# Kernel optimization log

Measured on AMD Instinct MI355X. Metric: run time of the kernel, lower is better.

The kernel has to match this reference:

```python
import jax, jax.numpy as jnp
import numpy as np

N = 50000        # nodes
E = 1_600_000    # edges (avg degree 32)
DIN, DH, DOUT = 128, 128, 64
TAU = 0.5
EPS = 1e-12
BN_EPS = 1e-5


def _lin(key, din, dout):
    kw, kb = jax.random.split(key)
    s = 1.0 / np.sqrt(din)
    W = jax.random.uniform(kw, (din, dout), jnp.float32, -s, s)
    b = jax.random.uniform(kb, (dout,), jnp.float32, -s, s)
    return W, b


def setup_inputs() -> dict:
    key = jax.random.key(0)
    ks = jax.random.split(key, 12)
    x = jax.random.normal(ks[0], (N, DIN), jnp.float32)
    edge_index = jax.random.randint(ks[1], (2, E), 0, N, dtype=jnp.int32).astype(jnp.int64)
    Wn0, cn0 = _lin(ks[2], DIN, DH)
    Wr0, cr0 = _lin(ks[3], DIN, DH)
    Wn1, cn1 = _lin(ks[4], DH, DH)
    Wr1, cr1 = _lin(ks[5], DH, DH)
    Wn2, cn2 = _lin(ks[6], DH, DOUT)
    Wr2, cr2 = _lin(ks[7], DH, DOUT)
    g0 = jnp.ones((DH,), jnp.float32); b0 = jnp.zeros((DH,), jnp.float32)
    m0 = 0.1 * jax.random.normal(ks[8], (DH,), jnp.float32)
    v0 = jax.random.uniform(ks[9], (DH,), jnp.float32, 0.5, 1.5)
    g1 = jnp.ones((DH,), jnp.float32); b1 = jnp.zeros((DH,), jnp.float32)
    m1 = 0.1 * jax.random.normal(ks[10], (DH,), jnp.float32)
    v1 = jax.random.uniform(ks[11], (DH,), jnp.float32, 0.5, 1.5)
    return dict(x=x, edge_index=edge_index,
                Wn0=Wn0, cn0=cn0, Wr0=Wr0, cr0=cr0,
                Wn1=Wn1, cn1=cn1, Wr1=Wr1, cr1=cr1,
                Wn2=Wn2, cn2=cn2, Wr2=Wr2, cr2=cr2,
                g0=g0, b0=b0, m0=m0, v0=v0,
                g1=g1, b1=b1, m1=m1, v1=v1)


def _edge_weights(x_sim, src, dst):
    # cosine similarity per edge, then softmax over incoming edges of each dst
    xn = x_sim / (jnp.linalg.norm(x_sim, axis=-1, keepdims=True) + EPS)
    sim = jnp.sum(xn[src] * xn[dst], axis=-1)            # [E]
    logits = sim / max(TAU, EPS)
    m = jax.ops.segment_max(logits, dst, num_segments=N)
    m = jnp.where(jnp.isfinite(m), m, 0.0)               # empty segments
    e = jnp.exp(logits - m[dst])
    denom = jax.ops.segment_sum(e, dst, num_segments=N)
    return e / (denom[dst] + 1e-16)


def _conv(x, src, dst, w, Wn, cn, Wr, cr):
    # gather x[src], scale by edge weight, scatter-add into dst
    agg = jax.ops.segment_sum(x[src] * w[:, None], dst, num_segments=N)  # [N, d]
    return agg @ Wn + cn + x @ Wr + cr


def _bn_eval(h, g, b, m, v):
    return (h - m) * (g / jnp.sqrt(v + BN_EPS)) + b


def reference(x, edge_index, Wn0, cn0, Wr0, cr0, Wn1, cn1, Wr1, cr1,
              Wn2, cn2, Wr2, cr2, g0, b0, m0, v0, g1, b1, m1, v1):
    src, dst = edge_index[0], edge_index[1]
    w = _edge_weights(x, src, dst)
    h = _conv(x, src, dst, w, Wn0, cn0, Wr0, cr0)
    h = jax.nn.relu(_bn_eval(h, g0, b0, m0, v0))
    h = _conv(h, src, dst, w, Wn1, cn1, Wr1, cr1)
    h = jax.nn.relu(_bn_eval(h, g1, b1, m1, v1))
    return _conv(h, src, dst, w, Wn2, cn2, Wr2, cr2)
```

## Files before the change

kernel.cpp:

```cpp
#include <hip/hip_runtime.h>
#include <hip/hip_fp16.h>
#include <hip/hip_fp8.h>
#include <math.h>
#include <type_traits>

#define N_NODES 50000
#define E_EDGES 1600000
#define TAU     0.5f
#define BN_EPS  1e-5f
#define SBSH    9
#define NSB     ((N_NODES + 511) >> 9)
#define NSUBL   8
#define SUBCAP  2560
#define BINCAP  48
#define EPB     1024
#define SCGRID  ((E_EDGES + EPB - 1) / EPB)
#define BSTR    16

typedef _Float16 f16x8 __attribute__((ext_vector_type(8)));
typedef float    f32x4 __attribute__((ext_vector_type(4)));
typedef float    f32x2 __attribute__((ext_vector_type(2)));

__device__ __forceinline__ f32x2 pk_fma(f32x2 a, f32x2 b, f32x2 c) {
  f32x2 d;
  asm volatile("v_pk_fma_f32 %0, %1, %2, %3"
               : "=v"(d) : "v"(a), "v"(b), "v"(c));
  return d;
}

__device__ __forceinline__ float dot16_fp8(int4 a, int4 b) {
  unsigned wa[4] = {(unsigned)a.x, (unsigned)a.y, (unsigned)a.z, (unsigned)a.w};
  unsigned wb[4] = {(unsigned)b.x, (unsigned)b.y, (unsigned)b.z, (unsigned)b.w};
  float acc = 0.0f;
  #pragma unroll
  for (int i = 0; i < 4; ++i) {
    f32x2 alo = __builtin_amdgcn_cvt_pk_f32_fp8(wa[i], false);
    f32x2 ahi = __builtin_amdgcn_cvt_pk_f32_fp8(wa[i], true);
    f32x2 blo = __builtin_amdgcn_cvt_pk_f32_fp8(wb[i], false);
    f32x2 bhi = __builtin_amdgcn_cvt_pk_f32_fp8(wb[i], true);
    acc = fmaf(alo[0], blo[0], acc);
    acc = fmaf(alo[1], blo[1], acc);
    acc = fmaf(ahi[0], bhi[0], acc);
    acc = fmaf(ahi[1], bhi[1], acc);
  }
  return acc;
}

__global__ __launch_bounds__(256) void xn_norm(
    const float* __restrict__ x, unsigned char* __restrict__ xn8, int n) {
  int wid  = (int)((blockIdx.x * blockDim.x + threadIdx.x) >> 6);
  int lane = threadIdx.x & 63;
  if (wid >= n) return;
  float2 v = ((const float2*)(x + (size_t)wid * 128))[lane];
  float s = v.x * v.x + v.y * v.y;
  #pragma unroll
  for (int off = 32; off; off >>= 1) s += __shfl_xor(s, off);
  float inv = 1.0f / (sqrtf(s) + 1e-12f);
  __hip_fp8_e4m3 q0(v.x * inv), q1(v.y * inv);
  uchar2 pk;
  pk.x = q0.__x; pk.y = q1.__x;
  ((uchar2*)(xn8 + (size_t)wid * 128))[lane] = pk;
}

__global__ __launch_bounds__(256) void scatter_sb(
    const int* __restrict__ src, const int* __restrict__ dst,
    int* __restrict__ gc, unsigned* __restrict__ staging,
    int* __restrict__ ocnt, unsigned* __restrict__ ostage, int e) {
  __shared__ unsigned bins[NSB][BINCAP];
  __shared__ int bcount[NSB];
  const int tid  = threadIdx.x;
  const int wv   = tid >> 6;
  const int lane = tid & 63;
  const int sl   = blockIdx.x & (NSUBL - 1);
  for (int i = tid; i < NSB; i += 256) bcount[i] = 0;
  __syncthreads();

  int base = blockIdx.x * EPB;
  int bend = min(base + EPB, e);
  for (int i = base + tid; i < bend; i += 256) {
    int d = dst[i], s = src[i];
    int sb = d >> SBSH;
    int pos = atomicAdd(&bcount[sb], 1);
    if (pos < BINCAP) {
      bins[sb][pos] = (unsigned)s | ((unsigned)(d & 511) << 16);
    } else {
      int op = atomicAdd(ocnt, 1);
      ostage[op] = (unsigned)s | ((unsigned)d << 16);
    }
  }
  __syncthreads();

  for (int sb = wv; sb < NSB; sb += 4) {
    int cnt = min(bcount[sb], BINCAP);
    if (cnt > 0) {
      int cell = sb * NSUBL + sl;
      int gbase = 0;
      if (lane == 0) gbase = atomicAdd(&gc[cell * BSTR], cnt);
      gbase = __shfl(gbase, 0);
      if (gbase + cnt <= SUBCAP) {
        if (lane < cnt)
          staging[(size_t)cell * SUBCAP + gbase + lane] = bins[sb][lane];
      } else if (lane < cnt) {
        unsigned u = bins[sb][lane];
        int op = atomicAdd(ocnt, 1);
        ostage[op] = (u & 0xFFFFu) | ((unsigned)((sb << SBSH) | (u >> 16)) << 16);
      }
    }
  }
}

__global__ __launch_bounds__(256) void hist_sb(
    const unsigned* __restrict__ staging, const int* __restrict__ gc,
    int* __restrict__ deg, int* __restrict__ sbsum, int n) {
  __shared__ int h[512];
  __shared__ int wt[4];
  int sb = blockIdx.x;
  for (int i = threadIdx.x; i < 512; i += 256) h[i] = 0;
  __syncthreads();
  for (int s = 0; s < NSUBL; ++s) {
    int cell = sb * NSUBL + s;
    int m = min(gc[cell * BSTR], SUBCAP);
    for (int i = threadIdx.x; i < m; i += 256)
      atomicAdd(&h[(staging[(size_t)cell * SUBCAP + i] >> 16) & 511], 1);
  }
  __syncthreads();
  int d0 = sb << SBSH;
  for (int i = threadIdx.x; i < 512; i += 256)
    if (d0 + i < n) deg[d0 + i] = h[i];
  int t = h[threadIdx.x] + h[threadIdx.x + 256];
  #pragma unroll
  for (int off = 32; off; off >>= 1) t += __shfl_xor(t, off);
  if ((threadIdx.x & 63) == 0) wt[threadIdx.x >> 6] = t;
  __syncthreads();
  if (threadIdx.x == 0) sbsum[sb] = wt[0] + wt[1] + wt[2] + wt[3];
}

__global__ __launch_bounds__(256) void overflow_deg(
    const unsigned* __restrict__ ostage, const int* __restrict__ ocnt,
    int* __restrict__ deg, int* __restrict__ sbsum) {
  int m = *ocnt;
  for (int i = blockIdx.x * blockDim.x + threadIdx.x; i < m;
       i += gridDim.x * blockDim.x) {
    int d = (int)(ostage[i] >> 16);
    atomicAdd(&deg[d], 1);
    atomicAdd(&sbsum[d >> SBSH], 1);
  }
}

__global__ void scan_sb(const int* __restrict__ sbsum, int* __restrict__ sbbase,
                        int* __restrict__ rowptr, int n) {
  __shared__ int part[128];
  int t = (int)threadIdx.x;
  int v = (t < NSB) ? sbsum[t] : 0;
  part[t] = v;
  __syncthreads();
  for (int off = 1; off < 128; off <<= 1) {
    int u = (t >= off) ? part[t - off] : 0;
    __syncthreads();
    part[t] += u;
    __syncthreads();
  }
  if (t < NSB) sbbase[t] = part[t] - v;
  if (t == 127) rowptr[n] = part[127];
}

__global__ __launch_bounds__(256) void rowptr_sb(
    const int* __restrict__ deg, const int* __restrict__ sbbase,
    int* __restrict__ rowptr, int n) {
  __shared__ int part[256];
  int sb = blockIdx.x;
  int d0 = sb << SBSH;
  int t = (int)threadIdx.x;
  int e0 = d0 + 2 * t;
  int v0 = (e0 < n) ? deg[e0] : 0;
  int v1 = (e0 + 1 < n) ? deg[e0 + 1] : 0;
  int s = v0 + v1;
  part[t] = s;
  __syncthreads();
  for (int off = 1; off < 256; off <<= 1) {
    int u = (t >= off) ? part[t - off] : 0;
    __syncthreads();
    part[t] += u;
    __syncthreads();
  }
  int ex = part[t] - s + sbbase[sb];
  if (e0 < n) rowptr[e0] = ex;
  if (e0 + 1 < n) rowptr[e0 + 1] = ex + v0;
}

__global__ __launch_bounds__(256) void place_sb(
    const unsigned* __restrict__ staging, const int* __restrict__ gc,
    const int* __restrict__ rowptr, unsigned short* __restrict__ csr16,
    int* __restrict__ gcur, int n) {
  __shared__ int cur[512];
  int sb = blockIdx.x;
  int d0 = sb << SBSH;
  for (int i = threadIdx.x; i < 512; i += 256)
    cur[i] = (d0 + i < n) ? rowptr[d0 + i] : 0;
  __syncthreads();
  for (int s = 0; s < NSUBL; ++s) {
    int cell = sb * NSUBL + s;
    int m = min(gc[cell * BSTR], SUBCAP);
    for (int i = threadIdx.x; i < m; i += 256) {
      unsigned u = staging[(size_t)cell * SUBCAP + i];
      int j = (u >> 16) & 511;
      int pos = atomicAdd(&cur[j], 1);
      csr16[pos] = (unsigned short)(u & 0xFFFFu);
    }
  }
  __syncthreads();
  for (int i = threadIdx.x; i < 512; i += 256)
    if (d0 + i < n) gcur[d0 + i] = cur[i];
}

__global__ __launch_bounds__(256) void overflow_place(
    const unsigned* __restrict__ ostage, const int* __restrict__ ocnt,
    int* __restrict__ gcur, unsigned short* __restrict__ csr16) {
  int m = *ocnt;
  for (int i = blockIdx.x * blockDim.x + threadIdx.x; i < m;
       i += gridDim.x * blockDim.x) {
    unsigned u = ostage[i];
    int d = (int)(u >> 16);
    int pos = atomicAdd(&gcur[d], 1);
    csr16[pos] = (unsigned short)(u & 0xFFFFu);
  }
}

__global__ __launch_bounds__(256) void edge_weights(
    const unsigned char* __restrict__ xn8, const int* __restrict__ rowptr,
    const unsigned short* __restrict__ csr_src16,
    unsigned* __restrict__ csrp, float* __restrict__ denom, int n) {
  int wid  = (int)((blockIdx.x * blockDim.x + threadIdx.x) >> 6);
  int lane = threadIdx.x & 63;
  if (wid >= n) return;
  int grp = lane >> 3;
  int sub = lane & 7;
  int beg = rowptr[wid], end = rowptr[wid + 1];
  int4 xdv = ((const int4*)(xn8 + (size_t)wid * 128))[sub];
  float wsum = 0.0f;

  for (int base = beg; base < end; base += 64) {
    int m = min(64, end - base);
    int sv = (lane < m) ? (int)csr_src16[base + lane] : 0;
    int iters = (m + 7) >> 3;
    #pragma unroll 2
    for (int q = 0; q < iters; ++q) {
      int ei = q * 8 + grp;
      int s = __shfl(sv, ei);
      int4 xsv = ((const int4*)(xn8 + (size_t)s * 128))[sub];
      float dp = dot16_fp8(xsv, xdv);
      dp += __shfl_xor(dp, 1);
      dp += __shfl_xor(dp, 2);
      dp += __shfl_xor(dp, 4);
      bool valid = ei < m;
      float w = valid ? __expf(dp * (1.0f / TAU)) : 0.0f;
      wsum += w;
      if (valid && sub == 0) {
        unsigned w16 = (unsigned)__half_as_ushort(__float2half_rn(w));
        csrp[base + ei] = (unsigned)s | (w16 << 16);
      }
    }
  }
  wsum += __shfl_xor(wsum, 8);
  wsum += __shfl_xor(wsum, 16);
  wsum += __shfl_xor(wsum, 32);
  if (lane == 0) denom[wid] = wsum;
}

__global__ __launch_bounds__(256) void prep_weights(
    const float* __restrict__ Wn0, const float* __restrict__ Wr0,
    const float* __restrict__ Wn1, const float* __restrict__ Wr1,
    const float* __restrict__ Wn2, const float* __restrict__ Wr2,
    const float* __restrict__ cn0, const float* __restrict__ cr0,
    const float* __restrict__ cn1, const float* __restrict__ cr1,
    const float* __restrict__ cn2, const float* __restrict__ cr2,
    __half* __restrict__ WtN0, __half* __restrict__ WtR0,
    __half* __restrict__ WtN1, __half* __restrict__ WtR1,
    __half* __restrict__ WtN2, __half* __restrict__ WtR2,
    float* __restrict__ bias0, float* __restrict__ bias1,
    float* __restrict__ bias2) {
  int i = blockIdx.x * blockDim.x + threadIdx.x;
  const float* Ws[6] = {Wn0, Wr0, Wn1, Wr1, Wn2, Wr2};
  __half*     Wts[6] = {WtN0, WtR0, WtN1, WtR1, WtN2, WtR2};
  int seg = -1, off = 0;
  if (i < 65536)        { seg = i >> 14;               off = i & 16383; }
  else if (i < 81920)   { int j = i - 65536; seg = 4 + (j >> 13); off = j & 8191; }
  if (seg >= 0) {
    int DO = (seg < 4) ? 128 : 64;
    int c = off >> 7, k = off & 127;
    int t = c >> 4, kc = k >> 5, kgrp = (k >> 3) & 3, j = k & 7;
    int lane = (c & 15) | (kgrp << 4);
    int idx = (((t * 4 + kc) * 64 + lane) << 3) + j;
    Wts[seg][idx] = __float2half_rn(Ws[seg][(size_t)k * DO + c]);
  }
  if (i < 128) { bias0[i] = cn0[i] + cr0[i]; bias1[i] = cn1[i] + cr1[i]; }
  if (i < 64)  { bias2[i] = cn2[i] + cr2[i]; }
}

template <int DO, typename TIN, int YMODE>
__global__ __launch_bounds__(256) void gemm_dual_mfma(
    const TIN* __restrict__ H, const __half* __restrict__ WfN,
    const __half* __restrict__ WfR, const float* __restrict__ bias,
    void* __restrict__ Yv, __half* __restrict__ Z, int n) {
  constexpr int NT = DO / 16;
  const int lane  = threadIdx.x & 63;
  const int w     = threadIdx.x >> 6;
  const int row0  = blockIdx.x * 64 + w * 16;
  const int col16 = lane & 15;
  const int kgrp  = (lane >> 4) * 8;
  const size_t arow = (size_t)min(row0 + col16, n - 1);

  f32x4 acc[2][NT];
  #pragma unroll
  for (int m = 0; m < 2; ++m)
    #pragma unroll
    for (int t = 0; t < NT; ++t) acc[m][t] = (f32x4){0.f, 0.f, 0.f, 0.f};

  #pragma unroll
  for (int kc = 0; kc < 4; ++kc) {
    f16x8 a;
    if constexpr (std::is_same<TIN, float>::value) {
      const float* hp = H + arow * 128 + kc * 32 + kgrp;
      float4 f0 = *(const float4*)hp;
      float4 f1 = *(const float4*)(hp + 4);
      a[0] = (_Float16)f0.x; a[1] = (_Float16)f0.y;
      a[2] = (_Float16)f0.z; a[3] = (_Float16)f0.w;
      a[4] = (_Float16)f1.x; a[5] = (_Float16)f1.y;
      a[6] = (_Float16)f1.z; a[7] = (_Float16)f1.w;
    } else {
      a = *(const f16x8*)(H + arow * 128 + kc * 32 + kgrp);
    }
    const f16x8* bN = (const f16x8*)(WfN + ((size_t)(kc * 64 + lane) << 3));
    const f16x8* bR = (const f16x8*)(WfR + ((size_t)(kc * 64 + lane) << 3));
    #pragma unroll
    for (int t = 0; t < NT; ++t) {
      f16x8 b = bN[t * 256];
      acc[0][t] = __builtin_amdgcn_mfma_f32_16x16x32_f16(a, b, acc[0][t], 0, 0, 0);
    }
    #pragma unroll
    for (int t = 0; t < NT; ++t) {
      f16x8 b = bR[t * 256];
      acc[1][t] = __builtin_amdgcn_mfma_f32_16x16x32_f16(a, b, acc[1][t], 0, 0, 0);
    }
  }

  const int rbase = (lane >> 4) * 4;
  #pragma unroll
  for (int t = 0; t < NT; ++t) {
    int col = t * 16 + col16;
    float bz = bias[col];
    #pragma unroll
    for (int j = 0; j < 4; ++j) {
      int row = row0 + rbase + j;
      if (row < n) {
        if constexpr (YMODE == 1) {
          __hip_fp8_e4m3 q(acc[0][t][j]);
          ((unsigned char*)Yv)[(size_t)row * DO + col] = q.__x;
        } else {
          ((__half*)Yv)[(size_t)row * DO + col] = __float2half_rn(acc[0][t][j]);
        }
        Z[(size_t)row * DO + col] = __float2half_rn(acc[1][t][j] + bz);
      }
    }
  }
}

template <bool DO_BN, bool HALF_OUT, bool FP8Y>
__global__ __launch_bounds__(256) void agg_pass(
    const void* __restrict__ Ypv, const __half* __restrict__ Zb,
    const int* __restrict__ rowptr, const unsigned* __restrict__ csrp,
    const float* __restrict__ denom,
    const float* __restrict__ g, const float* __restrict__ bb,
    const float* __restrict__ mm, const float* __restrict__ vv,
    void* __restrict__ outv, int dofull, int n) {
  constexpr int CH  = FP8Y ? 16 : 8;
  constexpr int CH2 = CH / 2;
  int wid  = (int)((blockIdx.x * blockDim.x + threadIdx.x) >> 6);
  int lane = threadIdx.x & 63;
  if (wid >= n) return;
  int grp = lane >> 3;
  int sub = lane & 7;
  int beg = rowptr[wid], end = rowptr[wid + 1];
  float inv = 1.0f / (denom[wid] + 1e-16f);

  f32x2 a2[CH2];
  #pragma unroll
  for (int k = 0; k < CH2; ++k) a2[k] = (f32x2){0.f, 0.f};

  for (int base = beg; base < end; base += 64) {
    int m = min(64, end - base);
    unsigned pk = (lane < m) ? csrp[base + lane] : 0u;
    int iters = (m + 7) >> 3;
    #pragma unroll 4
    for (int q = 0; q < iters; ++q) {
      unsigned u = __shfl(pk, q * 8 + grp);
      int   s = (int)(u & 0xFFFFu);
      float w = __half2float(__ushort_as_half((unsigned short)(u >> 16)));
      f32x2 w2 = {w, w};
      if constexpr (FP8Y) {
        int4 raw = ((const int4*)((const unsigned char*)Ypv +
                                  (size_t)s * 128))[sub];
        unsigned ww[4] = {(unsigned)raw.x, (unsigned)raw.y,
                          (unsigned)raw.z, (unsigned)raw.w};
        #pragma unroll
        for (int wi = 0; wi < 4; ++wi) {
          f32x2 lo = __builtin_amdgcn_cvt_pk_f32_fp8(ww[wi], false);
          f32x2 hi = __builtin_amdgcn_cvt_pk_f32_fp8(ww[wi], true);
          a2[wi * 2 + 0] = pk_fma(w2, lo, a2[wi * 2 + 0]);
          a2[wi * 2 + 1] = pk_fma(w2, hi, a2[wi * 2 + 1]);
        }
      } else {
        int4 raw = ((const int4*)((const __half*)Ypv + (size_t)s * 64))[sub];
        const __half2* hh = (const __half2*)&raw;
        #pragma unroll
        for (int k = 0; k < 4; ++k) {
          float2 f = __half22float2(hh[k]);
          f32x2 fv = {f.x, f.y};
          a2[k] = pk_fma(w2, fv, a2[k]);
        }
      }
    }
  }
  #pragma unroll
  for (int off = 8; off <= 32; off <<= 1) {
    #pragma unroll
    for (int k = 0; k < CH2; ++k) {
      a2[k][0] += __shfl_xor(a2[k][0], off);
      a2[k][1] += __shfl_xor(a2[k][1], off);
    }
  }

  if (lane < 8) {
    int c = sub * CH;
    float o[CH];
    const int4* zp = (const int4*)(Zb + (size_t)wid * dofull + c);
    #pragma unroll
    for (int v = 0; v < CH / 8; ++v) {
      int4 zr = zp[v];
      const __half2* zh = (const __half2*)&zr;
      #pragma unroll
      for (int k = 0; k < 4; ++k) {
        float2 z = __half22float2(zh[k]);
        o[v * 8 + 2 * k]     = fmaf(a2[v * 4 + k][0], inv, z.x);
        o[v * 8 + 2 * k + 1] = fmaf(a2[v * 4 + k][1], inv, z.y);
      }
    }
    if constexpr (DO_BN) {
      #pragma unroll
      for (int k = 0; k < CH; ++k) {
        float sc = g[c + k] * rsqrtf(vv[c + k] + BN_EPS);
        o[k] = fmaxf(fmaf(o[k] - mm[c + k], sc, bb[c + k]), 0.0f);
      }
    }
    if constexpr (HALF_OUT) {
      #pragma unroll
      for (int v = 0; v < CH / 8; ++v) {
        __half2 p0 = __floats2half2_rn(o[v * 8 + 0], o[v * 8 + 1]);
        __half2 p1 = __floats2half2_rn(o[v * 8 + 2], o[v * 8 + 3]);
        __half2 p2 = __floats2half2_rn(o[v * 8 + 4], o[v * 8 + 5]);
        __half2 p3 = __floats2half2_rn(o[v * 8 + 6], o[v * 8 + 7]);
        int4 pk4;
        pk4.x = *(int*)&p0; pk4.y = *(int*)&p1;
        pk4.z = *(int*)&p2; pk4.w = *(int*)&p3;
        ((int4*)((__half*)outv + (size_t)wid * dofull + c))[v] = pk4;
      }
    } else {
      float* op = (float*)outv + (size_t)wid * dofull + c;
      #pragma unroll
      for (int v = 0; v < CH / 4; ++v)
        ((float4*)op)[v] = make_float4(o[v * 4], o[v * 4 + 1],
                                       o[v * 4 + 2], o[v * 4 + 3]);
    }
  }
}

extern "C" void kernel_launch(void* const* d_in, const int* in_sizes, int n_in,
                              void* d_out, int out_size, void* d_ws, size_t ws_size,
                              hipStream_t stream) {
  const float* x   = (const float*)d_in[0];
  const int*   ei  = (const int*)d_in[1];
  const float* Wn0 = (const float*)d_in[2];
  const float* cn0 = (const float*)d_in[3];
  const float* Wr0 = (const float*)d_in[4];
  const float* cr0 = (const float*)d_in[5];
  const float* Wn1 = (const float*)d_in[6];
  const float* cn1 = (const float*)d_in[7];
  const float* Wr1 = (const float*)d_in[8];
  const float* cr1 = (const float*)d_in[9];
  const float* Wn2 = (const float*)d_in[10];
  const float* cn2 = (const float*)d_in[11];
  const float* Wr2 = (const float*)d_in[12];
  const float* cr2 = (const float*)d_in[13];
  const float* g0  = (const float*)d_in[14];
  const float* b0  = (const float*)d_in[15];
  const float* m0  = (const float*)d_in[16];
  const float* v0  = (const float*)d_in[17];
  const float* g1  = (const float*)d_in[18];
  const float* b1  = (const float*)d_in[19];
  const float* m1  = (const float*)d_in[20];
  const float* v1  = (const float*)d_in[21];

  const int* src = ei;
  const int* dst = ei + E_EDGES;

  char* p = (char*)d_ws;
  auto alloc = [&](size_t bytes) {
    char* r = p;
    p += (bytes + 255) & ~(size_t)255;
    return r;
  };
  __half*         P0      = (__half*)        alloc((size_t)N_NODES * 128 * 2);
  __half*         P1      = (__half*)        alloc((size_t)N_NODES * 128 * 2);
  __half*         A16     = (__half*)        alloc((size_t)N_NODES * 128 * 2);
  unsigned*       staging = (unsigned*)      alloc((size_t)NSB * NSUBL * SUBCAP * 4);
  int*            deg     = (int*)           alloc((size_t)N_NODES * 4);
  float*          denom   = (float*)         alloc((size_t)N_NODES * 4);
  int*            rowptr  = (int*)           alloc((size_t)(N_NODES + 1) * 4);
  int*            gcur    = (int*)           alloc((size_t)N_NODES * 4);
  int*            sbsum   = (int*)           alloc((size_t)NSB * 4);
  int*            sbbase  = (int*)           alloc((size_t)NSB * 4);
  int*            gc      = (int*)           alloc((size_t)(NSB * NSUBL * BSTR + 16) * 4);
  unsigned short* csrs16  = (unsigned short*)alloc((size_t)E_EDGES * 2);
  unsigned*       csrp    = (unsigned*)      alloc((size_t)E_EDGES * 4);
  __half*         WtN0    = (__half*)        alloc(128 * 128 * 2);
  __half*         WtR0    = (__half*)        alloc(128 * 128 * 2);
  __half*         WtN1    = (__half*)        alloc(128 * 128 * 2);
  __half*         WtR1    = (__half*)        alloc(128 * 128 * 2);
  __half*         WtN2    = (__half*)        alloc(64 * 128 * 2);
  __half*         WtR2    = (__half*)        alloc(64 * 128 * 2);
  float*          bias0   = (float*)         alloc(128 * 4);
  float*          bias1   = (float*)         alloc(128 * 4);
  float*          bias2   = (float*)         alloc(64 * 4);

  unsigned char* xn8 = (unsigned char*)P0;
  unsigned char* Y8  = (unsigned char*)P0;
  __half*        Yf  = P0;

  unsigned* ostage = (unsigned*)csrp;
  int*      ocnt   = gc + NSB * NSUBL * BSTR;

  hipMemsetAsync(gc, 0, (size_t)(NSB * NSUBL * BSTR + 16) * 4, stream);

  const int node_grid = (N_NODES * 64 + 255) / 256;

  xn_norm<<<node_grid, 256, 0, stream>>>(x, xn8, N_NODES);
  prep_weights<<<320, 256, 0, stream>>>(Wn0, Wr0, Wn1, Wr1, Wn2, Wr2,
                                        cn0, cr0, cn1, cr1, cn2, cr2,
                                        WtN0, WtR0, WtN1, WtR1, WtN2, WtR2,
                                        bias0, bias1, bias2);
  scatter_sb<<<SCGRID, 256, 0, stream>>>(src, dst, gc, staging, ocnt, ostage, E_EDGES);
  hist_sb<<<NSB, 256, 0, stream>>>(staging, gc, deg, sbsum, N_NODES);
  overflow_deg<<<64, 256, 0, stream>>>(ostage, ocnt, deg, sbsum);
  scan_sb<<<1, 128, 0, stream>>>(sbsum, sbbase, rowptr, N_NODES);
  rowptr_sb<<<NSB, 256, 0, stream>>>(deg, sbbase, rowptr, N_NODES);
  place_sb<<<NSB, 256, 0, stream>>>(staging, gc, rowptr, csrs16, gcur, N_NODES);
  overflow_place<<<64, 256, 0, stream>>>(ostage, ocnt, gcur, csrs16);
  edge_weights<<<node_grid, 256, 0, stream>>>(xn8, rowptr, csrs16, csrp, denom, N_NODES);

  const int gemm_grid = (N_NODES + 63) / 64;

  gemm_dual_mfma<128, float, 1><<<gemm_grid, 256, 0, stream>>>(
      x, WtN0, WtR0, bias0, Y8, P1, N_NODES);
  agg_pass<true, true, true><<<node_grid, 256, 0, stream>>>(
      Y8, P1, rowptr, csrp, denom, g0, b0, m0, v0, A16, 128, N_NODES);

  gemm_dual_mfma<128, __half, 1><<<gemm_grid, 256, 0, stream>>>(
      A16, WtN1, WtR1, bias1, Y8, P1, N_NODES);
  agg_pass<true, true, true><<<node_grid, 256, 0, stream>>>(
      Y8, P1, rowptr, csrp, denom, g1, b1, m1, v1, A16, 128, N_NODES);

  gemm_dual_mfma<64, __half, 0><<<gemm_grid, 256, 0, stream>>>(
      A16, WtN2, WtR2, bias2, Yf, P1, N_NODES);
  agg_pass<false, false, false><<<node_grid, 256, 0, stream>>>(
      Yf, P1, rowptr, csrp, denom,
      nullptr, nullptr, nullptr, nullptr, d_out, 64, N_NODES);
}
```

Baseline: 357.3 us.

## Fuse edge-weight computation into the first aggregation pass

```diff
diff --git a/kernel.cpp b/kernel.cpp
--- a/kernel.cpp
+++ b/kernel.cpp
@@ -226,10 +226,14 @@
   }
 }
 
-__global__ __launch_bounds__(256) void edge_weights(
-    const unsigned char* __restrict__ xn8, const int* __restrict__ rowptr,
+__global__ __launch_bounds__(256) void fused_ew_agg0(
+    const unsigned char* __restrict__ xn8, const unsigned char* __restrict__ Y8,
+    const __half* __restrict__ Zb, const int* __restrict__ rowptr,
     const unsigned short* __restrict__ csr_src16,
-    unsigned* __restrict__ csrp, float* __restrict__ denom, int n) {
+    unsigned* __restrict__ csrp, float* __restrict__ denom,
+    const float* __restrict__ g, const float* __restrict__ bb,
+    const float* __restrict__ mm, const float* __restrict__ vv,
+    __half* __restrict__ outv, int n) {
   int wid  = (int)((blockIdx.x * blockDim.x + threadIdx.x) >> 6);
   int lane = threadIdx.x & 63;
   if (wid >= n) return;
@@ -238,6 +242,10 @@
   int beg = rowptr[wid], end = rowptr[wid + 1];
   int4 xdv = ((const int4*)(xn8 + (size_t)wid * 128))[sub];
   float wsum = 0.0f;
+
+  f32x2 a2[8];
+  #pragma unroll
+  for (int k = 0; k < 8; ++k) a2[k] = (f32x2){0.f, 0.f};
 
   for (int base = beg; base < end; base += 64) {
     int m = min(64, end - base);
@@ -259,12 +267,66 @@
         unsigned w16 = (unsigned)__half_as_ushort(__float2half_rn(w));
         csrp[base + ei] = (unsigned)s | (w16 << 16);
       }
+      int4 raw = ((const int4*)(Y8 + (size_t)s * 128))[sub];
+      unsigned ww[4] = {(unsigned)raw.x, (unsigned)raw.y,
+                        (unsigned)raw.z, (unsigned)raw.w};
+      f32x2 w2 = {w, w};
+      #pragma unroll
+      for (int wi = 0; wi < 4; ++wi) {
+        f32x2 lo = __builtin_amdgcn_cvt_pk_f32_fp8(ww[wi], false);
+        f32x2 hi = __builtin_amdgcn_cvt_pk_f32_fp8(ww[wi], true);
+        a2[wi * 2 + 0] = pk_fma(w2, lo, a2[wi * 2 + 0]);
+        a2[wi * 2 + 1] = pk_fma(w2, hi, a2[wi * 2 + 1]);
+      }
     }
   }
   wsum += __shfl_xor(wsum, 8);
   wsum += __shfl_xor(wsum, 16);
   wsum += __shfl_xor(wsum, 32);
   if (lane == 0) denom[wid] = wsum;
+  float inv = 1.0f / (wsum + 1e-16f);
+
+  #pragma unroll
+  for (int off = 8; off <= 32; off <<= 1) {
+    #pragma unroll
+    for (int k = 0; k < 8; ++k) {
+      a2[k][0] += __shfl_xor(a2[k][0], off);
+      a2[k][1] += __shfl_xor(a2[k][1], off);
+    }
+  }
+
+  if (lane < 8) {
+    int c = sub * 16;
+    float o[16];
+    const int4* zp = (const int4*)(Zb + (size_t)wid * 128 + c);
+    #pragma unroll
+    for (int v = 0; v < 2; ++v) {
+      int4 zr = zp[v];
+      const __half2* zh = (const __half2*)&zr;
+      #pragma unroll
+      for (int k = 0; k < 4; ++k) {
+        float2 z = __half22float2(zh[k]);
+        o[v * 8 + 2 * k]     = fmaf(a2[v * 4 + k][0], inv, z.x);
+        o[v * 8 + 2 * k + 1] = fmaf(a2[v * 4 + k][1], inv, z.y);
+      }
+    }
+    #pragma unroll
+    for (int k = 0; k < 16; ++k) {
+      float sc = g[c + k] * rsqrtf(vv[c + k] + BN_EPS);
+      o[k] = fmaxf(fmaf(o[k] - mm[c + k], sc, bb[c + k]), 0.0f);
+    }
+    #pragma unroll
+    for (int v = 0; v < 2; ++v) {
+      __half2 p0 = __floats2half2_rn(o[v * 8 + 0], o[v * 8 + 1]);
+      __half2 p1 = __floats2half2_rn(o[v * 8 + 2], o[v * 8 + 3]);
+      __half2 p2 = __floats2half2_rn(o[v * 8 + 4], o[v * 8 + 5]);
+      __half2 p3 = __floats2half2_rn(o[v * 8 + 6], o[v * 8 + 7]);
+      int4 pk4;
+      pk4.x = *(int*)&p0; pk4.y = *(int*)&p1;
+      pk4.z = *(int*)&p2; pk4.w = *(int*)&p3;
+      ((int4*)(outv + (size_t)wid * 128 + c))[v] = pk4;
+    }
+  }
 }
 
 __global__ __launch_bounds__(256) void prep_weights(
@@ -533,7 +595,7 @@
   float*          bias2   = (float*)         alloc(64 * 4);
 
   unsigned char* xn8 = (unsigned char*)P0;
-  unsigned char* Y8  = (unsigned char*)P0;
+  unsigned char* Y8  = (unsigned char*)staging;
   __half*        Yf  = P0;
 
   unsigned* ostage = (unsigned*)csrp;
@@ -555,14 +617,14 @@
   rowptr_sb<<<NSB, 256, 0, stream>>>(deg, sbbase, rowptr, N_NODES);
   place_sb<<<NSB, 256, 0, stream>>>(staging, gc, rowptr, csrs16, gcur, N_NODES);
   overflow_place<<<64, 256, 0, stream>>>(ostage, ocnt, gcur, csrs16);
-  edge_weights<<<node_grid, 256, 0, stream>>>(xn8, rowptr, csrs16, csrp, denom, N_NODES);
 
   const int gemm_grid = (N_NODES + 63) / 64;
 
   gemm_dual_mfma<128, float, 1><<<gemm_grid, 256, 0, stream>>>(
       x, WtN0, WtR0, bias0, Y8, P1, N_NODES);
-  agg_pass<true, true, true><<<node_grid, 256, 0, stream>>>(
-      Y8, P1, rowptr, csrp, denom, g0, b0, m0, v0, A16, 128, N_NODES);
+  fused_ew_agg0<<<node_grid, 256, 0, stream>>>(
+      xn8, Y8, P1, rowptr, csrs16, csrp, denom,
+      g0, b0, m0, v0, A16, N_NODES);
 
   gemm_dual_mfma<128, __half, 1><<<gemm_grid, 256, 0, stream>>>(
       A16, WtN1, WtR1, bias1, Y8, P1, N_NODES);
```

Result: no change. 350.4 us (-1.9%).

## Aggregate before transform and fuse layer-0 aggregation into edge-weight kernel

Applied to the files above, without the earlier changes.

```diff
diff --git a/kernel.cpp b/kernel.cpp
--- a/kernel.cpp
+++ b/kernel.cpp
@@ -47,7 +47,8 @@
 }
 
 __global__ __launch_bounds__(256) void xn_norm(
-    const float* __restrict__ x, unsigned char* __restrict__ xn8, int n) {
+    const float* __restrict__ x, unsigned char* __restrict__ xn8,
+    float* __restrict__ norms, int n) {
   int wid  = (int)((blockIdx.x * blockDim.x + threadIdx.x) >> 6);
   int lane = threadIdx.x & 63;
   if (wid >= n) return;
@@ -55,11 +56,13 @@
   float s = v.x * v.x + v.y * v.y;
   #pragma unroll
   for (int off = 32; off; off >>= 1) s += __shfl_xor(s, off);
-  float inv = 1.0f / (sqrtf(s) + 1e-12f);
+  float sc = sqrtf(s) + 1e-12f;
+  float inv = 1.0f / sc;
   __hip_fp8_e4m3 q0(v.x * inv), q1(v.y * inv);
   uchar2 pk;
   pk.x = q0.__x; pk.y = q1.__x;
   ((uchar2*)(xn8 + (size_t)wid * 128))[lane] = pk;
+  if (lane == 0) norms[wid] = sc;
 }
 
 __global__ __launch_bounds__(256) void scatter_sb(
@@ -226,10 +229,11 @@
   }
 }
 
-__global__ __launch_bounds__(256) void edge_weights(
-    const unsigned char* __restrict__ xn8, const int* __restrict__ rowptr,
-    const unsigned short* __restrict__ csr_src16,
-    unsigned* __restrict__ csrp, float* __restrict__ denom, int n) {
+__global__ __launch_bounds__(256) void fused_ew_agg0(
+    const unsigned char* __restrict__ xn8, const float* __restrict__ norms,
+    const int* __restrict__ rowptr, const unsigned short* __restrict__ csr_src16,
+    unsigned* __restrict__ csrp, float* __restrict__ denom,
+    __half* __restrict__ aggX, int n) {
   int wid  = (int)((blockIdx.x * blockDim.x + threadIdx.x) >> 6);
   int lane = threadIdx.x & 63;
   if (wid >= n) return;
@@ -238,6 +242,10 @@
   int beg = rowptr[wid], end = rowptr[wid + 1];
   int4 xdv = ((const int4*)(xn8 + (size_t)wid * 128))[sub];
   float wsum = 0.0f;
+
+  f32x2 a2[8];
+  #pragma unroll
+  for (int k = 0; k < 8; ++k) a2[k] = (f32x2){0.f, 0.f};
 
   for (int base = beg; base < end; base += 64) {
     int m = min(64, end - base);
@@ -259,12 +267,108 @@
         unsigned w16 = (unsigned)__half_as_ushort(__float2half_rn(w));
         csrp[base + ei] = (unsigned)s | (w16 << 16);
       }
+      float ws = w * norms[s];
+      f32x2 w2 = {ws, ws};
+      unsigned ww[4] = {(unsigned)xsv.x, (unsigned)xsv.y,
+                        (unsigned)xsv.z, (unsigned)xsv.w};
+      #pragma unroll
+      for (int wi = 0; wi < 4; ++wi) {
+        f32x2 lo = __builtin_amdgcn_cvt_pk_f32_fp8(ww[wi], false);
+        f32x2 hi = __builtin_amdgcn_cvt_pk_f32_fp8(ww[wi], true);
+        a2[wi * 2 + 0] = pk_fma(w2, lo, a2[wi * 2 + 0]);
+        a2[wi * 2 + 1] = pk_fma(w2, hi, a2[wi * 2 + 1]);
+      }
     }
   }
   wsum += __shfl_xor(wsum, 8);
   wsum += __shfl_xor(wsum, 16);
   wsum += __shfl_xor(wsum, 32);
   if (lane == 0) denom[wid] = wsum;
+
+  #pragma unroll
+  for (int off = 8; off <= 32; off <<= 1) {
+    #pragma unroll
+    for (int k = 0; k < 8; ++k) {
+      a2[k][0] += __shfl_xor(a2[k][0], off);
+      a2[k][1] += __shfl_xor(a2[k][1], off);
+    }
+  }
+
+  if (lane < 8) {
+    int c = sub * 16;
+    #pragma unroll
+    for (int v = 0; v < 2; ++v) {
+      __half2 p0 = __floats2half2_rn(a2[v * 4 + 0][0], a2[v * 4 + 0][1]);
+      __half2 p1 = __floats2half2_rn(a2[v * 4 + 1][0], a2[v * 4 + 1][1]);
+      __half2 p2 = __floats2half2_rn(a2[v * 4 + 2][0], a2[v * 4 + 2][1]);
+      __half2 p3 = __floats2half2_rn(a2[v * 4 + 3][0], a2[v * 4 + 3][1]);
+      int4 pk4;
+      pk4.x = *(int*)&p0; pk4.y = *(int*)&p1;
+      pk4.z = *(int*)&p2; pk4.w = *(int*)&p3;
+      ((int4*)(aggX + (size_t)wid * 128 + c))[v] = pk4;
+    }
+  }
+}
+
+__global__ __launch_bounds__(256) void agg_h8(
+    const unsigned char* __restrict__ H8, const int* __restrict__ rowptr,
+    const unsigned* __restrict__ csrp, __half* __restrict__ aggH, int n) {
+  int wid  = (int)((blockIdx.x * blockDim.x + threadIdx.x) >> 6);
+  int lane = threadIdx.x & 63;
+  if (wid >= n) return;
+  int grp = lane >> 3;
+  int sub = lane & 7;
+  int beg = rowptr[wid], end = rowptr[wid + 1];
+
+  f32x2 a2[8];
+  #pragma unroll
+  for (int k = 0; k < 8; ++k) a2[k] = (f32x2){0.f, 0.f};
+
+  for (int base = beg; base < end; base += 64) {
+    int m = min(64, end - base);
+    unsigned pk = (lane < m) ? csrp[base + lane] : 0u;
+    int iters = (m + 7) >> 3;
+    #pragma unroll 4
+    for (int q = 0; q < iters; ++q) {
+      unsigned u = __shfl(pk, q * 8 + grp);
+      int   s = (int)(u & 0xFFFFu);
+      float w = __half2float(__ushort_as_half((unsigned short)(u >> 16)));
+      f32x2 w2 = {w, w};
+      int4 raw = ((const int4*)(H8 + (size_t)s * 128))[sub];
+      unsigned ww[4] = {(unsigned)raw.x, (unsigned)raw.y,
+                        (unsigned)raw.z, (unsigned)raw.w};
+      #pragma unroll
+      for (int wi = 0; wi < 4; ++wi) {
+        f32x2 lo = __builtin_amdgcn_cvt_pk_f32_fp8(ww[wi], false);
+        f32x2 hi = __builtin_amdgcn_cvt_pk_f32_fp8(ww[wi], true);
+        a2[wi * 2 + 0] = pk_fma(w2, lo, a2[wi * 2 + 0]);
+        a2[wi * 2 + 1] = pk_fma(w2, hi, a2[wi * 2 + 1]);
+      }
+    }
+  }
+  #pragma unroll
+  for (int off = 8; off <= 32; off <<= 1) {
+    #pragma unroll
+    for (int k = 0; k < 8; ++k) {
+      a2[k][0] += __shfl_xor(a2[k][0], off);
+      a2[k][1] += __shfl_xor(a2[k][1], off);
+    }
+  }
+
+  if (lane < 8) {
+    int c = sub * 16;
+    #pragma unroll
+    for (int v = 0; v < 2; ++v) {
+      __half2 p0 = __floats2half2_rn(a2[v * 4 + 0][0], a2[v * 4 + 0][1]);
+      __half2 p1 = __floats2half2_rn(a2[v * 4 + 1][0], a2[v * 4 + 1][1]);
+      __half2 p2 = __floats2half2_rn(a2[v * 4 + 2][0], a2[v * 4 + 2][1]);
+      __half2 p3 = __floats2half2_rn(a2[v * 4 + 3][0], a2[v * 4 + 3][1]);
+      int4 pk4;
+      pk4.x = *(int*)&p0; pk4.y = *(int*)&p1;
+      pk4.z = *(int*)&p2; pk4.w = *(int*)&p3;
+      ((int4*)(aggH + (size_t)wid * 128 + c))[v] = pk4;
+    }
+  }
 }
 
 __global__ __launch_bounds__(256) void prep_weights(
@@ -297,11 +401,14 @@
   if (i < 64)  { bias2[i] = cn2[i] + cr2[i]; }
 }
 
-template <int DO, typename TIN, int YMODE>
-__global__ __launch_bounds__(256) void gemm_dual_mfma(
-    const TIN* __restrict__ H, const __half* __restrict__ WfN,
-    const __half* __restrict__ WfR, const float* __restrict__ bias,
-    void* __restrict__ Yv, __half* __restrict__ Z, int n) {
+template <int DO, typename TIN1, bool DO_BN>
+__global__ __launch_bounds__(256) void gemm_post(
+    const __half* __restrict__ Agg, const TIN1* __restrict__ H,
+    const __half* __restrict__ WfN, const __half* __restrict__ WfR,
+    const float* __restrict__ bias, const float* __restrict__ denom,
+    const float* __restrict__ g, const float* __restrict__ bb,
+    const float* __restrict__ mm, const float* __restrict__ vv,
+    void* __restrict__ outH, unsigned char* __restrict__ outH8, int n) {
   constexpr int NT = DO / 16;
   const int lane  = threadIdx.x & 63;
   const int w     = threadIdx.x >> 6;
@@ -318,158 +425,65 @@
 
   #pragma unroll
   for (int kc = 0; kc < 4; ++kc) {
-    f16x8 a;
-    if constexpr (std::is_same<TIN, float>::value) {
+    f16x8 a0 = *(const f16x8*)(Agg + arow * 128 + kc * 32 + kgrp);
+    f16x8 a1;
+    if constexpr (std::is_same<TIN1, float>::value) {
       const float* hp = H + arow * 128 + kc * 32 + kgrp;
       float4 f0 = *(const float4*)hp;
       float4 f1 = *(const float4*)(hp + 4);
-      a[0] = (_Float16)f0.x; a[1] = (_Float16)f0.y;
-      a[2] = (_Float16)f0.z; a[3] = (_Float16)f0.w;
-      a[4] = (_Float16)f1.x; a[5] = (_Float16)f1.y;
-      a[6] = (_Float16)f1.z; a[7] = (_Float16)f1.w;
+      a1[0] = (_Float16)f0.x; a1[1] = (_Float16)f0.y;
+      a1[2] = (_Float16)f0.z; a1[3] = (_Float16)f0.w;
+      a1[4] = (_Float16)f1.x; a1[5] = (_Float16)f1.y;
+      a1[6] = (_Float16)f1.z; a1[7] = (_Float16)f1.w;
     } else {
-      a = *(const f16x8*)(H + arow * 128 + kc * 32 + kgrp);
+      a1 = *(const f16x8*)(H + arow * 128 + kc * 32 + kgrp);
     }
     const f16x8* bN = (const f16x8*)(WfN + ((size_t)(kc * 64 + lane) << 3));
     const f16x8* bR = (const f16x8*)(WfR + ((size_t)(kc * 64 + lane) << 3));
     #pragma unroll
     for (int t = 0; t < NT; ++t) {
       f16x8 b = bN[t * 256];
-      acc[0][t] = __builtin_amdgcn_mfma_f32_16x16x32_f16(a, b, acc[0][t], 0, 0, 0);
+      acc[0][t] = __builtin_amdgcn_mfma_f32_16x16x32_f16(a0, b, acc[0][t], 0, 0, 0);
     }
     #pragma unroll
     for (int t = 0; t < NT; ++t) {
       f16x8 b = bR[t * 256];
-      acc[1][t] = __builtin_amdgcn_mfma_f32_16x16x32_f16(a, b, acc[1][t], 0, 0, 0);
+      acc[1][t] = __builtin_amdgcn_mfma_f32_16x16x32_f16(a1, b, acc[1][t], 0, 0, 0);
     }
   }
 
   const int rbase = (lane >> 4) * 4;
+  float invd[4];
+  #pragma unroll
+  for (int j = 0; j < 4; ++j) {
+    int row = row0 + rbase + j;
+    invd[j] = 1.0f / (denom[min(row, n - 1)] + 1e-16f);
+  }
+
   #pragma unroll
   for (int t = 0; t < NT; ++t) {
     int col = t * 16 + col16;
     float bz = bias[col];
+    float sc = 0.f, sm = 0.f, sb2 = 0.f;
+    if constexpr (DO_BN) {
+      sc = g[col] * rsqrtf(vv[col] + BN_EPS);
+      sm = mm[col];
+      sb2 = bb[col];
+    }
     #pragma unroll
     for (int j = 0; j < 4; ++j) {
       int row = row0 + rbase + j;
       if (row < n) {
-        if constexpr (YMODE == 1) {
-          __hip_fp8_e4m3 q(acc[0][t][j]);
-          ((unsigned char*)Yv)[(size_t)row * DO + col] = q.__x;
+        float o = fmaf(acc[0][t][j], invd[j], acc[1][t][j] + bz);
+        if constexpr (DO_BN) {
+          o = fmaxf(fmaf(o - sm, sc, sb2), 0.0f);
+          ((__half*)outH)[(size_t)row * DO + col] = __float2half_rn(o);
+          __hip_fp8_e4m3 q(o);
+          outH8[(size_t)row * DO + col] = q.__x;
         } else {
-          ((__half*)Yv)[(size_t)row * DO + col] = __float2half_rn(acc[0][t][j]);
-        }
-        Z[(size_t)row * DO + col] = __float2half_rn(acc[1][t][j] + bz);
-      }
-    }
-  }
-}
-
-template <bool DO_BN, bool HALF_OUT, bool FP8Y>
-__global__ __launch_bounds__(256) void agg_pass(
-    const void* __restrict__ Ypv, const __half* __restrict__ Zb,
-    const int* __restrict__ rowptr, const unsigned* __restrict__ csrp,
-    const float* __restrict__ denom,
-    const float* __restrict__ g, const float* __restrict__ bb,
-    const float* __restrict__ mm, const float* __restrict__ vv,
-    void* __restrict__ outv, int dofull, int n) {
-  constexpr int CH  = FP8Y ? 16 : 8;
-  constexpr int CH2 = CH / 2;
-  int wid  = (int)((blockIdx.x * blockDim.x + threadIdx.x) >> 6);
-  int lane = threadIdx.x & 63;
-  if (wid >= n) return;
-  int grp = lane >> 3;
-  int sub = lane & 7;
-  int beg = rowptr[wid], end = rowptr[wid + 1];
-  float inv = 1.0f / (denom[wid] + 1e-16f);
-
-  f32x2 a2[CH2];
-  #pragma unroll
-  for (int k = 0; k < CH2; ++k) a2[k] = (f32x2){0.f, 0.f};
-
-  for (int base = beg; base < end; base += 64) {
-    int m = min(64, end - base);
-    unsigned pk = (lane < m) ? csrp[base + lane] : 0u;
-    int iters = (m + 7) >> 3;
-    #pragma unroll 4
-    for (int q = 0; q < iters; ++q) {
-      unsigned u = __shfl(pk, q * 8 + grp);
-      int   s = (int)(u & 0xFFFFu);
-      float w = __half2float(__ushort_as_half((unsigned short)(u >> 16)));
-      f32x2 w2 = {w, w};
-      if constexpr (FP8Y) {
-        int4 raw = ((const int4*)((const unsigned char*)Ypv +
-                                  (size_t)s * 128))[sub];
-        unsigned ww[4] = {(unsigned)raw.x, (unsigned)raw.y,
-                          (unsigned)raw.z, (unsigned)raw.w};
-        #pragma unroll
-        for (int wi = 0; wi < 4; ++wi) {
-          f32x2 lo = __builtin_amdgcn_cvt_pk_f32_fp8(ww[wi], false);
-          f32x2 hi = __builtin_amdgcn_cvt_pk_f32_fp8(ww[wi], true);
-          a2[wi * 2 + 0] = pk_fma(w2, lo, a2[wi * 2 + 0]);
-          a2[wi * 2 + 1] = pk_fma(w2, hi, a2[wi * 2 + 1]);
-        }
-      } else {
-        int4 raw = ((const int4*)((const __half*)Ypv + (size_t)s * 64))[sub];
-        const __half2* hh = (const __half2*)&raw;
-        #pragma unroll
-        for (int k = 0; k < 4; ++k) {
-          float2 f = __half22float2(hh[k]);
-          f32x2 fv = {f.x, f.y};
-          a2[k] = pk_fma(w2, fv, a2[k]);
+          ((float*)outH)[(size_t)row * DO + col] = o;
         }
       }
-    }
-  }
-  #pragma unroll
-  for (int off = 8; off <= 32; off <<= 1) {
-    #pragma unroll
-    for (int k = 0; k < CH2; ++k) {
-      a2[k][0] += __shfl_xor(a2[k][0], off);
-      a2[k][1] += __shfl_xor(a2[k][1], off);
-    }
-  }
-
-  if (lane < 8) {
-    int c = sub * CH;
-    float o[CH];
-    const int4* zp = (const int4*)(Zb + (size_t)wid * dofull + c);
-    #pragma unroll
-    for (int v = 0; v < CH / 8; ++v) {
-      int4 zr = zp[v];
-      const __half2* zh = (const __half2*)&zr;
-      #pragma unroll
-      for (int k = 0; k < 4; ++k) {
-        float2 z = __half22float2(zh[k]);
-        o[v * 8 + 2 * k]     = fmaf(a2[v * 4 + k][0], inv, z.x);
-        o[v * 8 + 2 * k + 1] = fmaf(a2[v * 4 + k][1], inv, z.y);
-      }
-    }
-    if constexpr (DO_BN) {
-      #pragma unroll
-      for (int k = 0; k < CH; ++k) {
-        float sc = g[c + k] * rsqrtf(vv[c + k] + BN_EPS);
-        o[k] = fmaxf(fmaf(o[k] - mm[c + k], sc, bb[c + k]), 0.0f);
-      }
-    }
-    if constexpr (HALF_OUT) {
-      #pragma unroll
-      for (int v = 0; v < CH / 8; ++v) {
-        __half2 p0 = __floats2half2_rn(o[v * 8 + 0], o[v * 8 + 1]);
-        __half2 p1 = __floats2half2_rn(o[v * 8 + 2], o[v * 8 + 3]);
-        __half2 p2 = __floats2half2_rn(o[v * 8 + 4], o[v * 8 + 5]);
-        __half2 p3 = __floats2half2_rn(o[v * 8 + 6], o[v * 8 + 7]);
-        int4 pk4;
-        pk4.x = *(int*)&p0; pk4.y = *(int*)&p1;
-        pk4.z = *(int*)&p2; pk4.w = *(int*)&p3;
-        ((int4*)((__half*)outv + (size_t)wid * dofull + c))[v] = pk4;
-      }
-    } else {
-      float* op = (float*)outv + (size_t)wid * dofull + c;
-      #pragma unroll
-      for (int v = 0; v < CH / 4; ++v)
-        ((float4*)op)[v] = make_float4(o[v * 4], o[v * 4 + 1],
-                                       o[v * 4 + 2], o[v * 4 + 3]);
     }
   }
 }
@@ -515,6 +529,7 @@
   unsigned*       staging = (unsigned*)      alloc((size_t)NSB * NSUBL * SUBCAP * 4);
   int*            deg     = (int*)           alloc((size_t)N_NODES * 4);
   float*          denom   = (float*)         alloc((size_t)N_NODES * 4);
+  float*          norms   = (float*)         alloc((size_t)N_NODES * 4);
   int*            rowptr  = (int*)           alloc((size_t)(N_NODES + 1) * 4);
   int*            gcur    = (int*)           alloc((size_t)N_NODES * 4);
   int*            sbsum   = (int*)           alloc((size_t)NSB * 4);
@@ -533,8 +548,8 @@
   float*          bias2   = (float*)         alloc(64 * 4);
 
   unsigned char* xn8 = (unsigned char*)P0;
-  unsigned char* Y8  = (unsigned char*)P0;
-  __half*        Yf  = P0;
+  unsigned char* H8  = (unsigned char*)staging;
+  __half*        H2  = P0;
 
   unsigned* ostage = (unsigned*)csrp;
   int*      ocnt   = gc + NSB * NSUBL * BSTR;
@@ -542,8 +557,9 @@
   hipMemsetAsync(gc, 0, (size_t)(NSB * NSUBL * BSTR + 16) * 4, stream);
 
   const int node_grid = (N_NODES * 64 + 255) / 256;
-
-  xn_norm<<<node_grid, 256, 0, stream>>>(x, xn8, N_NODES);
+  const int gemm_grid = (N_NODES + 63) / 64;
+
+  xn_norm<<<node_grid, 256, 0, stream>>>(x, xn8, norms, N_NODES);
   prep_weights<<<320, 256, 0, stream>>>(Wn0, Wr0, Wn1, Wr1, Wn2, Wr2,
                                         cn0, cr0, cn1, cr1, cn2, cr2,
                                         WtN0, WtR0, WtN1, WtR1, WtN2, WtR2,
@@ -555,23 +571,18 @@
   rowptr_sb<<<NSB, 256, 0, stream>>>(deg, sbbase, rowptr, N_NODES);
   place_sb<<<NSB, 256, 0, stream>>>(staging, gc, rowptr, csrs16, gcur, N_NODES);
   overflow_place<<<64, 256, 0, stream>>>(ostage, ocnt, gcur, csrs16);
-  edge_weights<<<node_grid, 256, 0, stream>>>(xn8, rowptr, csrs16, csrp, denom, N_NODES);
-
-  const int gemm_grid = (N_NODES + 63) / 64;
-
-  gemm_dual_mfma<128, float, 1><<<gemm_grid, 256, 0, stream>>>(
-      x, WtN0, WtR0, bias0, Y8, P1, N_NODES);
-  agg_pass<true, true, true><<<node_grid, 256, 0, stream>>>(
-      Y8, P1, rowptr, csrp, denom, g0, b0, m0, v0, A16, 128, N_NODES);
-
-  gemm_dual_mfma<128, __half, 1><<<gemm_grid, 256, 0, stream>>>(
-      A16, WtN1, WtR1, bias1, Y8, P1, N_NODES);
-  agg_pass<true, true, true><<<node_grid, 256, 0, stream>>>(
-      Y8, P1, rowptr, csrp, denom, g1, b1, m1, v1, A16, 128, N_NODES);
-
-  gemm_dual_mfma<64, __half, 0><<<gemm_grid, 256, 0, stream>>>(
-      A16, WtN2, WtR2, bias2, Yf, P1, N_NODES);
-  agg_pass<false, false, false><<<node_grid, 256, 0, stream>>>(
-      Yf, P1, rowptr, csrp, denom,
-      nullptr, nullptr, nullptr, nullptr, d_out, 64, N_NODES);
-}
+
+  fused_ew_agg0<<<node_grid, 256, 0, stream>>>(
+      xn8, norms, rowptr, csrs16, csrp, denom, P1, N_NODES);
+  gemm_post<128, float, true><<<gemm_grid, 256, 0, stream>>>(
+      P1, x, WtN0, WtR0, bias0, denom, g0, b0, m0, v0, A16, H8, N_NODES);
+
+  agg_h8<<<node_grid, 256, 0, stream>>>(H8, rowptr, csrp, P1, N_NODES);
+  gemm_post<128, __half, true><<<gemm_grid, 256, 0, stream>>>(
+      P1, A16, WtN1, WtR1, bias1, denom, g1, b1, m1, v1, H2, H8, N_NODES);
+
+  agg_h8<<<node_grid, 256, 0, stream>>>(H8, rowptr, csrp, P1, N_NODES);
+  gemm_post<64, __half, false><<<gemm_grid, 256, 0, stream>>>(
+      P1, H2, WtN2, WtR2, bias2, denom,
+      nullptr, nullptr, nullptr, nullptr, d_out, nullptr, N_NODES);
+}
```

Result: faster. 335.6 us (-6.1%).
